# Kernel optimization log

Hardware: AMD Instinct MI355X
Metric: run time of the kernel (lower is better)

The kernel has to match this reference:

```python
import jax, jax.numpy as jnp
import numpy as np

L = 768
Z_DIM = 128
C = 32
EPS = 1e-5


def _layer_norm(x, w, b):
    mu = jnp.mean(x, axis=-1, keepdims=True)
    var = jnp.mean(jnp.square(x - mu), axis=-1, keepdims=True)
    return (x - mu) * jax.lax.rsqrt(var + EPS) * w + b


def setup_inputs() -> dict:
    key = jax.random.key(0)
    ks = jax.random.split(key, 12)
    s_z = 1.0 / np.sqrt(Z_DIM)
    s_c = 1.0 / np.sqrt(C)
    return {
        "z": jax.random.normal(ks[0], (L, L, Z_DIM), dtype=jnp.float32),
        "norm_w": jnp.ones((Z_DIM,), jnp.float32),
        "norm_b": jnp.zeros((Z_DIM,), jnp.float32),
        "onorm_w": jnp.ones((C,), jnp.float32),
        "onorm_b": jnp.zeros((C,), jnp.float32),
        "a_w": jax.random.normal(ks[1], (C, Z_DIM), jnp.float32) * s_z,
        "a_b": jnp.zeros((C,), jnp.float32),
        "ag_w": jax.random.normal(ks[2], (C, Z_DIM), jnp.float32) * s_z,
        "ag_b": jnp.zeros((C,), jnp.float32),
        "g_w": jax.random.normal(ks[3], (Z_DIM, Z_DIM), jnp.float32) * s_z,
        "g_b": jnp.zeros((Z_DIM,), jnp.float32),
        "o_w": jax.random.normal(ks[4], (Z_DIM, C), jnp.float32) * s_c,
        "o_b": jnp.zeros((Z_DIM,), jnp.float32),
    }


def reference(z, norm_w, norm_b, onorm_w, onorm_b, a_w, a_b, ag_w, ag_b, g_w, g_b, o_w, o_b):
    zn = _layer_norm(z, norm_w, norm_b)                       # [L,L,Z]
    a = (zn @ a_w.T + a_b) * jax.nn.sigmoid(zn @ ag_w.T + ag_b)  # [L,L,C]
    # source computes b with the same (a) projections -> b == a
    o = jnp.einsum('ilc,jlc->ijc', a, a)                      # [L,L,C]
    o = _layer_norm(o, onorm_w, onorm_b)
    o = o @ o_w.T + o_b                                        # [L,L,Z]
    o = o * jax.nn.sigmoid(zn @ g_w.T + g_b)
    return o
```

## Files before the change

### kernel.cpp

```cpp
#include <hip/hip_runtime.h>
#include <math.h>


#define LDIM 768
#define LL   (768 * 768)
#define ZD   128
#define CD   32

typedef __bf16 bf16x8 __attribute__((ext_vector_type(8)));
typedef float  f32x4  __attribute__((ext_vector_type(4)));

__device__ __forceinline__ ushort f2bf(float f) {
    __bf16 h = (__bf16)f;
    return __builtin_bit_cast(ushort, h);
}
__device__ __forceinline__ float bf2f(ushort u) {
    return __builtin_bit_cast(float, ((unsigned)u) << 16);
}
__device__ __forceinline__ float sigm(float x) {
    return __builtin_amdgcn_rcpf(1.0f + __expf(-x));
}

__global__ __launch_bounds__(256) void k0_wfrag(
    const float* __restrict__ aw, const float* __restrict__ agw,
    const float* __restrict__ gw, const float* __restrict__ ow,
    ushort* __restrict__ wfrag, ushort* __restrict__ ofrag)
{
    const int idx = blockIdx.x * 256 + threadIdx.x;
    if (idx >= 3584) return;
    union { ushort us[8]; uint4 q; } pk;
    if (idx < 3072) {
        const int f = idx, n4 = f >> 6, lane = f & 63;
        const int n = n4 >> 2, kk = n4 & 3;
        const int fr = lane & 15, hi = lane >> 4;
        const int ch = n * 16 + fr;
        const int k0 = kk * 32 + hi * 8;
        const float* src = (ch < 32) ? (aw + ch * ZD)
                         : (ch < 64) ? (agw + (ch - 32) * ZD)
                                     : (gw + (ch - 64) * ZD);
        #pragma unroll
        for (int j = 0; j < 8; ++j) pk.us[j] = f2bf(src[k0 + j]);
        *(uint4*)&wfrag[(size_t)f * 8] = pk.q;
    } else {
        const int e = idx - 3072;
        const int n = e >> 6, lane = e & 63;
        const int fr = lane & 15, hi = lane >> 4;
        const float* src = ow + (n * 16 + fr) * CD + hi * 8;
        #pragma unroll
        for (int j = 0; j < 8; ++j) pk.us[j] = f2bf(src[j]);
        *(uint4*)&ofrag[(size_t)e * 8] = pk.q;
    }
}

__global__ __launch_bounds__(256) void k1_ln_proj(
    const float* __restrict__ z, const float* __restrict__ nw, const float* __restrict__ nb,
    const ushort* __restrict__ wfrag,
    const float* __restrict__ ab, const float* __restrict__ agb, const float* __restrict__ gb,
    ushort* __restrict__ a_t, ushort* __restrict__ gate)
{
    __shared__ ushort zn[64][136];
    __shared__ ushort gl[64][136];

    const int tid = threadIdx.x;
    const int lane = tid & 63, wave = tid >> 6;
    const int fr = lane & 15, hi = lane >> 4;

    const int t0 = (wave < 2) ? wave     : 6 + (wave - 2) * 3;
    const int t1 = (wave < 2) ? wave + 2 : t0 + 1;
    const int t2 = (wave < 2) ? wave + 4 : t0 + 2;

    bf16x8 bv0[4], bv1[4], bv2[4];
    {
        const ushort* wl = wfrag + (size_t)lane * 8;
        #pragma unroll
        for (int kk = 0; kk < 4; ++kk) {
            bv0[kk] = *(const bf16x8*)(wl + (size_t)(t0 * 4 + kk) * 512);
            bv1[kk] = *(const bf16x8*)(wl + (size_t)(t1 * 4 + kk) * 512);
            bv2[kk] = *(const bf16x8*)(wl + (size_t)(t2 * 4 + kk) * 512);
        }
    }

    float abv = 0.f, agbv = 0.f, gbv0 = 0.f, gbv1 = 0.f, gbv2;
    if (wave < 2) {
        abv  = ab[wave * 16 + fr];
        agbv = agb[wave * 16 + fr];
        gbv2 = gb[t2 * 16 - 64 + fr];
    } else {
        gbv0 = gb[t0 * 16 - 64 + fr];
        gbv1 = gb[t1 * 16 - 64 + fr];
        gbv2 = gb[t2 * 16 - 64 + fr];
    }

    const size_t blockrow = (size_t)blockIdx.x * 256;
    const int lr = tid >> 2, seg = tid & 3;

    float4 zreg[8];
    {
        const float4* zp = (const float4*)(z + (blockrow + lr) * ZD + seg * 32);
        #pragma unroll
        for (int q = 0; q < 8; ++q) zreg[q] = zp[q];
    }

    for (int c = 0; c < 4; ++c) {
        __syncthreads();

        {
            float v[32];
            #pragma unroll
            for (int q = 0; q < 8; ++q) {
                v[q * 4 + 0] = zreg[q].x; v[q * 4 + 1] = zreg[q].y;
                v[q * 4 + 2] = zreg[q].z; v[q * 4 + 3] = zreg[q].w;
            }
            float s = 0.f, ss = 0.f;
            #pragma unroll
            for (int e = 0; e < 32; ++e) { s += v[e]; ss += v[e] * v[e]; }
            s += __shfl_xor(s, 1); ss += __shfl_xor(ss, 1);
            s += __shfl_xor(s, 2); ss += __shfl_xor(ss, 2);
            const float mu  = s * (1.f / 128.f);
            const float var = ss * (1.f / 128.f) - mu * mu;
            const float rs  = rsqrtf(var + 1e-5f);
            union { ushort u[32]; uint4 q4[4]; } pk;
            #pragma unroll
            for (int e = 0; e < 32; ++e) {
                const int k = seg * 32 + e;
                pk.u[e] = f2bf((v[e] - mu) * rs * nw[k] + nb[k]);
            }
            #pragma unroll
            for (int q = 0; q < 4; ++q)
                *(uint4*)&zn[lr][seg * 32 + q * 8] = pk.q4[q];
        }

        if (c < 3) {
            const float4* zp = (const float4*)(z + (blockrow + (c + 1) * 64 + lr) * ZD + seg * 32);
            #pragma unroll
            for (int q = 0; q < 8; ++q) zreg[q] = zp[q];
        }
        __syncthreads();

        f32x4 acc0[4], acc1[4], acc2[4];
        #pragma unroll
        for (int m = 0; m < 4; ++m) {
            acc0[m] = (f32x4){0.f, 0.f, 0.f, 0.f};
            acc1[m] = (f32x4){0.f, 0.f, 0.f, 0.f};
            acc2[m] = (f32x4){0.f, 0.f, 0.f, 0.f};
        }
        #pragma unroll
        for (int m = 0; m < 4; ++m) {
            bf16x8 afm[4];
            #pragma unroll
            for (int kk = 0; kk < 4; ++kk)
                afm[kk] = *(const bf16x8*)&zn[m * 16 + fr][kk * 32 + hi * 8];
            #pragma unroll
            for (int kk = 0; kk < 4; ++kk) {
                acc0[m] = __builtin_amdgcn_mfma_f32_16x16x32_bf16(afm[kk], bv0[kk], acc0[m], 0, 0, 0);
                acc1[m] = __builtin_amdgcn_mfma_f32_16x16x32_bf16(afm[kk], bv1[kk], acc1[m], 0, 0, 0);
                acc2[m] = __builtin_amdgcn_mfma_f32_16x16x32_bf16(afm[kk], bv2[kk], acc2[m], 0, 0, 0);
            }
        }

        const size_t rb = blockrow + (size_t)c * 64;
        if (wave < 2) {
            const int ch = wave * 16 + fr;
            #pragma unroll
            for (int m = 0; m < 4; ++m) {
                union { ushort u[4]; uint2 d; } pk;
                #pragma unroll
                for (int q = 0; q < 4; ++q)
                    pk.u[q] = f2bf((acc0[m][q] + abv) * sigm(acc1[m][q] + agbv));
                *(uint2*)&a_t[(size_t)ch * LL + rb + m * 16 + hi * 4] = pk.d;
            }
            const int gch = t2 * 16 - 64 + fr;
            #pragma unroll
            for (int m = 0; m < 4; ++m)
                #pragma unroll
                for (int q = 0; q < 4; ++q)
                    gl[m * 16 + hi * 4 + q][gch] = f2bf(sigm(acc2[m][q] + gbv2));
        } else {
            const int g0 = t0 * 16 - 64 + fr;
            const int g1 = t1 * 16 - 64 + fr;
            const int g2 = t2 * 16 - 64 + fr;
            #pragma unroll
            for (int m = 0; m < 4; ++m)
                #pragma unroll
                for (int q = 0; q < 4; ++q) {
                    const int row = m * 16 + hi * 4 + q;
                    gl[row][g0] = f2bf(sigm(acc0[m][q] + gbv0));
                    gl[row][g1] = f2bf(sigm(acc1[m][q] + gbv1));
                    gl[row][g2] = f2bf(sigm(acc2[m][q] + gbv2));
                }
        }
        __syncthreads();

        #pragma unroll
        for (int it = 0; it < 4; ++it) {
            const int idx = it * 256 + tid;
            const int r = idx >> 4, cq = idx & 15;
            *(uint4*)&gate[(rb + r) * ZD + cq * 8] = *(const uint4*)&gl[r][cq * 8];
        }
    }
}

__global__ __launch_bounds__(256) void k2_einsum(
    const ushort* __restrict__ a_t, ushort* __restrict__ obuf16)
{
    __shared__ ushort As[2][64][32];
    __shared__ ushort Bs[2][64][32];

    const int tid = threadIdx.x;
    const int c = blockIdx.y;
    int p = blockIdx.x, bi = 0;
    while (p >= 12 - bi) { p -= 12 - bi; ++bi; }
    const int bj = bi + p;
    const int i0 = bi * 64, j0 = bj * 64;
    const ushort* base = a_t + (size_t)c * LL;

    const int srow = tid >> 2, scol = (tid & 3) * 8;
    const ushort* gA = base + (size_t)(i0 + srow) * LDIM + scol;
    const ushort* gB = base + (size_t)(j0 + srow) * LDIM + scol;

    const int wave = tid >> 6, lane = tid & 63;
    const int wi = (wave >> 1) * 32, wj = (wave & 1) * 32;
    const int fr = lane & 15, k8 = (lane >> 4) * 8;

    f32x4 acc[2][2];
    #pragma unroll
    for (int m = 0; m < 2; ++m)
        #pragma unroll
        for (int n = 0; n < 2; ++n)
            acc[m][n] = (f32x4){0.f, 0.f, 0.f, 0.f};

    auto stage = [&](int b, int kc) {
        __builtin_amdgcn_global_load_lds(
            (const uint*)(gA + kc * 32), (uint*)&As[b][srow][scol], 16, 0, 0);
        __builtin_amdgcn_global_load_lds(
            (const uint*)(gB + kc * 32), (uint*)&Bs[b][srow][scol], 16, 0, 0);
    };

    stage(0, 0);
    __syncthreads();
    for (int kc = 0; kc < 24; ++kc) {
        const int cur = kc & 1;
        if (kc + 1 < 24) stage(cur ^ 1, kc + 1);

        bf16x8 av[2], bv[2];
        #pragma unroll
        for (int m = 0; m < 2; ++m)
            av[m] = *(const bf16x8*)&As[cur][wi + m * 16 + fr][k8];
        #pragma unroll
        for (int n = 0; n < 2; ++n)
            bv[n] = *(const bf16x8*)&Bs[cur][wj + n * 16 + fr][k8];

        #pragma unroll
        for (int m = 0; m < 2; ++m)
            #pragma unroll
            for (int n = 0; n < 2; ++n)
                acc[m][n] = __builtin_amdgcn_mfma_f32_16x16x32_bf16(
                    av[m], bv[n], acc[m][n], 0, 0, 0);
        __syncthreads();
    }

    ushort* ob = obuf16 + (size_t)c * LL;
    #pragma unroll
    for (int m = 0; m < 2; ++m)
        #pragma unroll
        for (int n = 0; n < 2; ++n) {
            #pragma unroll
            for (int q = 0; q < 4; ++q) {
                const int row = i0 + wi + m * 16 + (lane >> 4) * 4 + q;
                const int col = j0 + wj + n * 16 + fr;
                ob[(size_t)row * LDIM + col] = f2bf(acc[m][n][q]);
            }
            if (bi != bj) {
                const int mrow = j0 + wj + n * 16 + fr;
                const int mcol = i0 + wi + m * 16 + (lane >> 4) * 4;
                union { ushort u[4]; uint2 d; } pk;
                #pragma unroll
                for (int q = 0; q < 4; ++q) pk.u[q] = f2bf(acc[m][n][q]);
                *(uint2*)&ob[(size_t)mrow * LDIM + mcol] = pk.d;
            }
        }
}

__global__ __launch_bounds__(256) void k3_out(
    const ushort* __restrict__ obuf16,
    const float* __restrict__ onw, const float* __restrict__ onb,
    const ushort* __restrict__ ofrag, const float* __restrict__ obias,
    const ushort* __restrict__ gate, float* __restrict__ out)
{
    __shared__ float  Ol[64][40];
    __shared__ ushort An[64][36];

    const int tid = threadIdx.x;
    const int lane = tid & 63, wave = tid >> 6;
    const int fr = lane & 15, hi = lane >> 4;
    const size_t rowbase = (size_t)blockIdx.x * 64;

    bf16x8 ofr[8];
    #pragma unroll
    for (int n = 0; n < 8; ++n)
        ofr[n] = *(const bf16x8*)&ofrag[(size_t)n * 512 + lane * 8];

    #pragma unroll
    for (int cc = 0; cc < 4; ++cc) {
        const int ch = wave * 8 + cc * 2 + (lane >> 5);
        const int r2 = (lane & 31) * 2;
        const uint uu = *(const uint*)&obuf16[(size_t)ch * LL + rowbase + r2];
        Ol[r2][ch]     = bf2f((ushort)(uu & 0xffff));
        Ol[r2 + 1][ch] = bf2f((ushort)(uu >> 16));
    }
    __syncthreads();

    {
        const int r = tid >> 2, seg = tid & 3;
        float v[8];
        #pragma unroll
        for (int e = 0; e < 8; ++e) v[e] = Ol[r][seg * 8 + e];
        float s = 0.f, ss = 0.f;
        #pragma unroll
        for (int e = 0; e < 8; ++e) { s += v[e]; ss += v[e] * v[e]; }
        s += __shfl_xor(s, 1); ss += __shfl_xor(ss, 1);
        s += __shfl_xor(s, 2); ss += __shfl_xor(ss, 2);
        const float mu  = s * (1.f / 32.f);
        const float var = ss * (1.f / 32.f) - mu * mu;
        const float rs  = rsqrtf(var + 1e-5f);
        union { ushort us[8]; uint4 q; } pk;
        #pragma unroll
        for (int e = 0; e < 8; ++e) {
            const int c = seg * 8 + e;
            pk.us[e] = f2bf((v[e] - mu) * rs * onw[c] + onb[c]);
        }
        *(uint4*)&An[r][seg * 8] = pk.q;
    }
    __syncthreads();

    const int wrow = wave * 16;
    const bf16x8 af = *(const bf16x8*)&An[wrow + fr][hi * 8];
    const size_t orow = rowbase + wrow + fr;

    #pragma unroll
    for (int n = 0; n < 8; ++n) {
        const f32x4 acc = __builtin_amdgcn_mfma_f32_16x16x32_bf16(
            ofr[n], af, (f32x4){0.f, 0.f, 0.f, 0.f}, 0, 0, 0);
        const int ch0 = n * 16 + hi * 4;
        const float4 ob4 = *(const float4*)&obias[ch0];
        union { uint2 d; ushort us[4]; } g;
        g.d = *(const uint2*)&gate[orow * ZD + ch0];
        float4 w;
        w.x = (acc[0] + ob4.x) * bf2f(g.us[0]);
        w.y = (acc[1] + ob4.y) * bf2f(g.us[1]);
        w.z = (acc[2] + ob4.z) * bf2f(g.us[2]);
        w.w = (acc[3] + ob4.w) * bf2f(g.us[3]);
        *(float4*)&out[orow * ZD + ch0] = w;
    }
}

extern "C" void kernel_launch(void* const* d_in, const int* in_sizes, int n_in,
                              void* d_out, int out_size, void* d_ws, size_t ws_size,
                              hipStream_t stream) {
    (void)in_sizes; (void)n_in; (void)out_size; (void)ws_size;
    const float* z   = (const float*)d_in[0];
    const float* nw  = (const float*)d_in[1];
    const float* nb  = (const float*)d_in[2];
    const float* onw = (const float*)d_in[3];
    const float* onb = (const float*)d_in[4];
    const float* aw  = (const float*)d_in[5];
    const float* ab  = (const float*)d_in[6];
    const float* agw = (const float*)d_in[7];
    const float* agb = (const float*)d_in[8];
    const float* gw  = (const float*)d_in[9];
    const float* gb  = (const float*)d_in[10];
    const float* ow  = (const float*)d_in[11];
    const float* ob  = (const float*)d_in[12];

    char* ws = (char*)d_ws;
    ushort* a_t    = (ushort*)ws;
    ushort* gate   = (ushort*)(ws + 37748736);
    ushort* obuf16 = (ushort*)(ws + 188743680);
    ushort* wfrag  = (ushort*)(ws + 226492416);
    ushort* ofrag  = (ushort*)(ws + 226541568);

    k0_wfrag<<<14, 256, 0, stream>>>(aw, agw, gw, ow, wfrag, ofrag);
    k1_ln_proj<<<LL / 256, 256, 0, stream>>>(z, nw, nb, wfrag, ab, agb, gb,
                                             a_t, gate);
    k2_einsum<<<dim3(78, 32), 256, 0, stream>>>(a_t, obuf16);
    k3_out<<<LL / 64, 256, 0, stream>>>(obuf16, onw, onb, ofrag, ob, gate,
                                        (float*)d_out);
}
```

Baseline: 299.3 us.

## Defer gate copy-out to overlap next chunk and coalesce output stores via LDS

In the projection kernel, the gate tile's copy from shared memory to global is deferred into the next iteration, after the layernorm write. This removes one barrier per chunk and lets the global stores overlap with compute. In the output kernel, the MFMA results plus bias are staged through a shared-memory buffer (unioned with the existing one) so that gate reads and output writes become fully coalesced row-contiguous float4 accesses. The cost is an extra barrier and more LDS traffic in the output kernel.

```diff
diff --git a/kernel.cpp b/kernel.cpp
--- a/kernel.cpp
+++ b/kernel.cpp
@@ -101,6 +101,16 @@
         for (int q = 0; q < 8; ++q) zreg[q] = zp[q];
     }
 
+    auto copy_out = [&](int cc) {
+        const size_t rbp = blockrow + (size_t)cc * 64;
+        #pragma unroll
+        for (int it = 0; it < 4; ++it) {
+            const int idx = it * 256 + tid;
+            const int r = idx >> 4, cq = idx & 15;
+            *(uint4*)&gate[(rbp + r) * ZD + cq * 8] = *(const uint4*)&gl[r][cq * 8];
+        }
+    };
+
     for (int c = 0; c < 4; ++c) {
         __syncthreads();
 
@@ -129,6 +139,8 @@
             for (int q = 0; q < 4; ++q)
                 *(uint4*)&zn[lr][seg * 32 + q * 8] = pk.q4[q];
         }
+
+        if (c > 0) copy_out(c - 1);
 
         if (c < 3) {
             const float4* zp = (const float4*)(z + (blockrow + (c + 1) * 64 + lr) * ZD + seg * 32);
@@ -189,15 +201,9 @@
                     gl[row][g2] = f2bf(sigm(acc2[m][q] + gbv2));
                 }
         }
-        __syncthreads();
-
-        #pragma unroll
-        for (int it = 0; it < 4; ++it) {
-            const int idx = it * 256 + tid;
-            const int r = idx >> 4, cq = idx & 15;
-            *(uint4*)&gate[(rb + r) * ZD + cq * 8] = *(const uint4*)&gl[r][cq * 8];
-        }
-    }
+    }
+    __syncthreads();
+    copy_out(3);
 }
 
 __global__ __launch_bounds__(256) void k2_einsum(
@@ -287,12 +293,11 @@
     const ushort* __restrict__ ofrag, const float* __restrict__ obias,
     const ushort* __restrict__ gate, float* __restrict__ out)
 {
-    __shared__ float  Ol[64][40];
+    __shared__ union { float Ol[64][40]; float Res[64][132]; } u;
     __shared__ ushort An[64][36];
 
     const int tid = threadIdx.x;
     const int lane = tid & 63, wave = tid >> 6;
-    const int fr = lane & 15, hi = lane >> 4;
     const size_t rowbase = (size_t)blockIdx.x * 64;
 
     bf16x8 ofr[8];
@@ -305,8 +310,8 @@
         const int ch = wave * 8 + cc * 2 + (lane >> 5);
         const int r2 = (lane & 31) * 2;
         const uint uu = *(const uint*)&obuf16[(size_t)ch * LL + rowbase + r2];
-        Ol[r2][ch]     = bf2f((ushort)(uu & 0xffff));
-        Ol[r2 + 1][ch] = bf2f((ushort)(uu >> 16));
+        u.Ol[r2][ch]     = bf2f((ushort)(uu & 0xffff));
+        u.Ol[r2 + 1][ch] = bf2f((ushort)(uu >> 16));
     }
     __syncthreads();
 
@@ -314,7 +319,7 @@
         const int r = tid >> 2, seg = tid & 3;
         float v[8];
         #pragma unroll
-        for (int e = 0; e < 8; ++e) v[e] = Ol[r][seg * 8 + e];
+        for (int e = 0; e < 8; ++e) v[e] = u.Ol[r][seg * 8 + e];
         float s = 0.f, ss = 0.f;
         #pragma unroll
         for (int e = 0; e < 8; ++e) { s += v[e]; ss += v[e] * v[e]; }
@@ -333,24 +338,36 @@
     }
     __syncthreads();
 
+    const int fr = lane & 15, hi = lane >> 4;
     const int wrow = wave * 16;
+
     const bf16x8 af = *(const bf16x8*)&An[wrow + fr][hi * 8];
-    const size_t orow = rowbase + wrow + fr;
+    f32x4 acc[8];
+    #pragma unroll
+    for (int n = 0; n < 8; ++n)
+        acc[n] = __builtin_amdgcn_mfma_f32_16x16x32_bf16(
+            af, ofr[n], (f32x4){0.f, 0.f, 0.f, 0.f}, 0, 0, 0);
 
     #pragma unroll
     for (int n = 0; n < 8; ++n) {
-        const f32x4 acc = __builtin_amdgcn_mfma_f32_16x16x32_bf16(
-            ofr[n], af, (f32x4){0.f, 0.f, 0.f, 0.f}, 0, 0, 0);
-        const int ch0 = n * 16 + hi * 4;
-        const float4 ob4 = *(const float4*)&obias[ch0];
+        const int ch = n * 16 + fr;
+        const float obv = obias[ch];
+        #pragma unroll
+        for (int q = 0; q < 4; ++q)
+            u.Res[wrow + hi * 4 + q][ch] = acc[n][q] + obv;
+    }
+    __syncthreads();
+
+    #pragma unroll
+    for (int it = 0; it < 8; ++it) {
+        const int idx = it * 256 + tid;
+        const int r = idx >> 5, cq = (idx & 31) * 4;
+        float4 v4 = *(const float4*)&u.Res[r][cq];
         union { uint2 d; ushort us[4]; } g;
-        g.d = *(const uint2*)&gate[orow * ZD + ch0];
-        float4 w;
-        w.x = (acc[0] + ob4.x) * bf2f(g.us[0]);
-        w.y = (acc[1] + ob4.y) * bf2f(g.us[1]);
-        w.z = (acc[2] + ob4.z) * bf2f(g.us[2]);
-        w.w = (acc[3] + ob4.w) * bf2f(g.us[3]);
-        *(float4*)&out[orow * ZD + ch0] = w;
+        g.d = *(const uint2*)&gate[(rowbase + r) * ZD + cq];
+        v4.x *= bf2f(g.us[0]); v4.y *= bf2f(g.us[1]);
+        v4.z *= bf2f(g.us[2]); v4.w *= bf2f(g.us[3]);
+        *(float4*)&out[(rowbase + r) * ZD + cq] = v4;
     }
 }
 
```

Result: faster. 277.0 us (-7.5%).
